# Performance work log

Hardware: AMD Instinct MI355X
Metric: run time of the kernel (lower is better)

## Reference

```python
import jax, jax.numpy as jnp
import numpy as np

NUM_USERS = 100_000
NUM_ITEMS = 50_000
EMBED_DIM = 64
NUM_LAYERS = 3
NUM_BASE_EDGES = 2_000_000
BATCH = 4096


def setup_inputs() -> dict:
    key = jax.random.key(0)
    k_ue, k_ie, k_u, k_i, k_uid, k_iid = jax.random.split(key, 6)
    N = NUM_USERS + NUM_ITEMS
    # learned embedding tables (std=0.01 init as in the torch module)
    user_emb = 0.01 * jax.random.normal(k_ue, (NUM_USERS, EMBED_DIM), dtype=jnp.float32)
    item_emb = 0.01 * jax.random.normal(k_ie, (NUM_ITEMS, EMBED_DIM), dtype=jnp.float32)
    # random bipartite interaction edges (u, v); symmetrized as in _build_graph
    u = jax.random.randint(k_u, (NUM_BASE_EDGES,), 0, NUM_USERS, dtype=jnp.int32)
    v = jax.random.randint(k_i, (NUM_BASE_EDGES,), 0, NUM_ITEMS, dtype=jnp.int32) + NUM_USERS
    rows = jnp.concatenate([u, v])  # [2E]
    cols = jnp.concatenate([v, u])  # [2E]
    # symmetric degree normalization: A_hat[r,c] = 1 / (sqrt(deg[r]) * sqrt(deg[c]))
    deg = jax.ops.segment_sum(jnp.ones_like(rows, dtype=jnp.float32), rows, num_segments=N)
    sqrt_deg = jnp.sqrt(deg)
    vals = 1.0 / (sqrt_deg[rows] * sqrt_deg[cols])
    user_ids = jax.random.randint(k_uid, (BATCH,), 0, NUM_USERS, dtype=jnp.int32)
    item_ids = jax.random.randint(k_iid, (BATCH,), 0, NUM_ITEMS, dtype=jnp.int32)
    return {
        "user_emb": user_emb,
        "item_emb": item_emb,
        "vals": vals,
        "rows": rows,
        "cols": cols,
        "user_ids": user_ids,
        "item_ids": item_ids,
    }


def _spmm(vals, rows, cols, x, num_segments):
    # COO SpMM: out[r] += vals[e] * x[cols[e]]  (irregular gather + scatter-add)
    return jax.ops.segment_sum(vals[:, None] * x[cols], rows, num_segments=num_segments)


def reference(user_emb, item_emb, vals, rows, cols, user_ids, item_ids):
    num_users = user_emb.shape[0]
    N = num_users + item_emb.shape[0]
    all_emb = jnp.concatenate([user_emb, item_emb], axis=0)  # [N, D]
    acc = jnp.zeros_like(all_emb)
    for _ in range(NUM_LAYERS):  # eval mode: no stochastic noise injection
        all_emb = _spmm(vals, rows, cols, all_emb, N)
        acc = acc + all_emb
    final = acc / NUM_LAYERS  # mean over layer outputs
    u = final[user_ids]                       # [B, D]
    i = final[item_ids + num_users]           # [B, D]
    return (u * i).sum(axis=-1)               # [B]
```

## Files before the change

kernel.cpp:

```cpp
#include <hip/hip_runtime.h>


#define EMBED_DIM 64
#define NUM_LAYERS 3
#define RSHIFT 8
#define RMASK 255
#define NBMAX 640
#define CAPU 8192
#define CAPI 12288
#define TP 3584
#define OUT_CAP 12288

__device__ __forceinline__ int bucket_base(int b, int BSPLIT) {
    int lo = (b < BSPLIT) ? b : BSPLIT;
    int hi = (b > BSPLIT) ? (b - BSPLIT) : 0;
    return lo * CAPU + hi * CAPI;
}


__device__ __forceinline__ unsigned bf16pair(float a, float b) {
    unsigned ia = __float_as_uint(a);
    unsigned ib = __float_as_uint(b);
    ia = (ia + 0x7fffu + ((ia >> 16) & 1u)) >> 16;
    ib = (ib + 0x7fffu + ((ib >> 16) & 1u)) & 0xffff0000u;
    return ia | ib;
}
__device__ __forceinline__ float bf_lo(unsigned u) { return __uint_as_float(u << 16); }
__device__ __forceinline__ float bf_hi(unsigned u) { return __uint_as_float(u & 0xffff0000u); }


__global__ __launch_bounds__(512) void split_kernel(const int* __restrict__ uu,
                                                    const int* __restrict__ vv,
                                                    int* __restrict__ gcur,
                                                    int* __restrict__ bin, int E2, int NB,
                                                    int BSPLIT) {
    __shared__ int h[NBMAX], exl[NBMAX], curb[NBMAX], gb[NBMAX];
    __shared__ int wp[8];
    __shared__ int stage[2 * TP];
    int tid = threadIdx.x;
    int lane = tid & 63, wid = tid >> 6;
    for (int i = tid; i < NB; i += 512) h[i] = 0;
    __syncthreads();
    int e0 = blockIdx.x * TP, e1 = min(e0 + TP, E2);
    int j = e0 + tid * 4;
    for (; j + 3 < e1; j += 2048) {
        int4 u4 = *(const int4*)(uu + j);
        int4 v4 = *(const int4*)(vv + j);
        atomicAdd(&h[u4.x >> RSHIFT], 1); atomicAdd(&h[v4.x >> RSHIFT], 1);
        atomicAdd(&h[u4.y >> RSHIFT], 1); atomicAdd(&h[v4.y >> RSHIFT], 1);
        atomicAdd(&h[u4.z >> RSHIFT], 1); atomicAdd(&h[v4.z >> RSHIFT], 1);
        atomicAdd(&h[u4.w >> RSHIFT], 1); atomicAdd(&h[v4.w >> RSHIFT], 1);
    }
    for (; j < e1; ++j) {
        atomicAdd(&h[uu[j] >> RSHIFT], 1);
        atomicAdd(&h[vv[j] >> RSHIFT], 1);
    }
    __syncthreads();
    {
        int b2 = tid * 2;
        int v0 = (b2     < NB) ? h[b2]     : 0;
        int v1 = (b2 + 1 < NB) ? h[b2 + 1] : 0;
        int tsum = v0 + v1;
        int x = tsum;
        for (int off = 1; off < 64; off <<= 1) {
            int y = __shfl_up(x, off, 64);
            if (lane >= off) x += y;
        }
        if (lane == 63) wp[wid] = x;
        __syncthreads();
        int wadd = 0;
        for (int k = 0; k < wid; ++k) wadd += wp[k];
        int tpre = wadd + x - tsum;
        if (b2     < NB) exl[b2]     = tpre;
        if (b2 + 1 < NB) exl[b2 + 1] = tpre + v0;
        __syncthreads();
    }
    for (int b = tid; b < NB; b += 512) {
        curb[b] = exl[b];
        gb[b]   = h[b] ? (bucket_base(b, BSPLIT) + atomicAdd(&gcur[b], h[b])) : 0;
    }
    __syncthreads();
    j = e0 + tid * 4;
    for (; j + 3 < e1; j += 2048) {
        int4 u4 = *(const int4*)(uu + j);
        int4 v4 = *(const int4*)(vv + j);
        int p;
        p = atomicAdd(&curb[u4.x >> RSHIFT], 1); stage[p] = (v4.x << RSHIFT) | (u4.x & RMASK);
        p = atomicAdd(&curb[v4.x >> RSHIFT], 1); stage[p] = (u4.x << RSHIFT) | (v4.x & RMASK);
        p = atomicAdd(&curb[u4.y >> RSHIFT], 1); stage[p] = (v4.y << RSHIFT) | (u4.y & RMASK);
        p = atomicAdd(&curb[v4.y >> RSHIFT], 1); stage[p] = (u4.y << RSHIFT) | (v4.y & RMASK);
        p = atomicAdd(&curb[u4.z >> RSHIFT], 1); stage[p] = (v4.z << RSHIFT) | (u4.z & RMASK);
        p = atomicAdd(&curb[v4.z >> RSHIFT], 1); stage[p] = (u4.z << RSHIFT) | (v4.z & RMASK);
        p = atomicAdd(&curb[u4.w >> RSHIFT], 1); stage[p] = (v4.w << RSHIFT) | (u4.w & RMASK);
        p = atomicAdd(&curb[v4.w >> RSHIFT], 1); stage[p] = (u4.w << RSHIFT) | (v4.w & RMASK);
    }
    for (; j < e1; ++j) {
        int u = uu[j], v = vv[j];
        int p1 = atomicAdd(&curb[u >> RSHIFT], 1);
        stage[p1] = (v << RSHIFT) | (u & RMASK);
        int p2 = atomicAdd(&curb[v >> RSHIFT], 1);
        stage[p2] = (u << RSHIFT) | (v & RMASK);
    }
    __syncthreads();
    int noct = tid >> 3, osub = tid & 7;
    for (int b = noct; b < NB; b += 64) {
        int cnt_b = h[b];
        int st = exl[b], g = gb[b];
        for (int k = osub; k < cnt_b; k += 8) bin[g + k] = stage[st + k];
    }
}


__global__ __launch_bounds__(512) void csr_kernel(const int* __restrict__ bin,
                                                  const int* __restrict__ gcur,
                                                  int* __restrict__ row_ptr,
                                                  int* __restrict__ deg,
                                                  int* __restrict__ col_idx,
                                                  const float4* __restrict__ ue,
                                                  const float4* __restrict__ ie,
                                                  unsigned* __restrict__ w0x,
                                                  int N, int U, int BSPLIT, int NB) {
    __shared__ int h2[256], cur2[256];
    __shared__ float rs2[256];
    __shared__ int wp[8];
    __shared__ __align__(16) int outst[OUT_CAP];
    int nbi = NB - BSPLIT;
    int bb  = blockIdx.x;
    int b   = (bb < nbi) ? (BSPLIT + bb) : (bb - nbi);
    int tid = threadIdx.x;
    int lane = tid & 63, wid = tid >> 6;
    int s = bucket_base(b, BSPLIT);
    int cnt = gcur[b];
    if (tid < 256) h2[tid] = 0;
    __syncthreads();
    int cnt4 = cnt >> 2;
    const int4* bin4 = (const int4*)(bin + s);
    for (int j = tid; j < cnt4; j += 512) {
        int4 v = bin4[j];
        atomicAdd(&h2[v.x & RMASK], 1);
        atomicAdd(&h2[v.y & RMASK], 1);
        atomicAdd(&h2[v.z & RMASK], 1);
        atomicAdd(&h2[v.w & RMASK], 1);
    }
    for (int j = (cnt4 << 2) + tid; j < cnt; j += 512) atomicAdd(&h2[bin[s + j] & RMASK], 1);
    __syncthreads();
    int myh = (tid < 256) ? h2[tid] : 0;
    if (tid < 256) rs2[tid] = (myh > 0) ? rsqrtf((float)myh) : 0.0f;
    {
        int x = myh;
        for (int off = 1; off < 64; off <<= 1) {
            int y = __shfl_up(x, off, 64);
            if (lane >= off) x += y;
        }
        if (lane == 63) wp[wid] = x;
        __syncthreads();
        if (tid < 256) {
            int wadd = 0;
            for (int k = 0; k < wid; ++k) wadd += wp[k];
            cur2[tid] = wadd + x - myh;
        }
    }
    int gr = (b << RSHIFT) + tid;
    if (tid < 256 && gr < N) {
        row_ptr[gr] = s + cur2[tid];
        deg[gr]     = myh;
    }
    __syncthreads();
    if (cnt <= OUT_CAP) {
        for (int j = tid; j < cnt4; j += 512) {
            int4 v = bin4[j];
            int p;
            p = atomicAdd(&cur2[v.x & RMASK], 1); outst[p] = v.x >> RSHIFT;
            p = atomicAdd(&cur2[v.y & RMASK], 1); outst[p] = v.y >> RSHIFT;
            p = atomicAdd(&cur2[v.z & RMASK], 1); outst[p] = v.z >> RSHIFT;
            p = atomicAdd(&cur2[v.w & RMASK], 1); outst[p] = v.w >> RSHIFT;
        }
        for (int j = (cnt4 << 2) + tid; j < cnt; j += 512) {
            int v = bin[s + j];
            int p = atomicAdd(&cur2[v & RMASK], 1);
            outst[p] = v >> RSHIFT;
        }
        __syncthreads();
        int4* dst4 = (int4*)(col_idx + s);
        for (int j = tid; j < cnt4; j += 512) dst4[j] = ((const int4*)outst)[j];
        for (int j = (cnt4 << 2) + tid; j < cnt; j += 512) col_idx[s + j] = outst[j];
    } else {
        for (int j = tid; j < cnt; j += 512) {
            int v = bin[s + j];
            int p = atomicAdd(&cur2[v & RMASK], 1);
            col_idx[s + p] = v >> RSHIFT;
        }
    }
    for (int idx = tid; idx < 256 * 16; idx += 512) {
        int rl = idx >> 4, sub = idx & 15;
        int n = (b << RSHIFT) + rl;
        if (n < N) {
            float4 v = (n < U) ? ue[(size_t)n * 16 + sub] : ie[(size_t)(n - U) * 16 + sub];
            float rs = rs2[rl];
            uint2 o;
            o.x = bf16pair(v.x * rs, v.y * rs);
            o.y = bf16pair(v.z * rs, v.w * rs);
            ((uint2*)w0x)[(size_t)n * 16 + sub] = o;
        }
    }
}


__global__ __launch_bounds__(256) void spmm_kernel(const int* __restrict__ row_ptr,
                                                   const int* __restrict__ deg,
                                                   const int* __restrict__ col_idx,
                                                   const uint4* __restrict__ x4,
                                                   uint4* __restrict__ y4, int N) {
    int gw   = (blockIdx.x * blockDim.x + threadIdx.x) >> 6;
    int lane = threadIdx.x & 63;
    int oct  = lane >> 3, sub = lane & 7;
    int r = gw * 8 + oct;
    if (r >= N) return;
    int s = row_ptr[r];
    int d = deg[r];
    float2 a0 = {0, 0}, a1 = {0, 0}, a2 = {0, 0}, a3 = {0, 0};
    int k = 0;
    for (; k + 3 < d; k += 4) {
        int c0 = col_idx[s + k];
        int c1 = col_idx[s + k + 1];
        int c2 = col_idx[s + k + 2];
        int c3 = col_idx[s + k + 3];
        uint4 u0 = x4[(size_t)c0 * 8 + sub];
        uint4 u1 = x4[(size_t)c1 * 8 + sub];
        uint4 u2 = x4[(size_t)c2 * 8 + sub];
        uint4 u3 = x4[(size_t)c3 * 8 + sub];
        a0.x += bf_lo(u0.x); a0.y += bf_hi(u0.x);
        a1.x += bf_lo(u0.y); a1.y += bf_hi(u0.y);
        a2.x += bf_lo(u0.z); a2.y += bf_hi(u0.z);
        a3.x += bf_lo(u0.w); a3.y += bf_hi(u0.w);
        a0.x += bf_lo(u1.x); a0.y += bf_hi(u1.x);
        a1.x += bf_lo(u1.y); a1.y += bf_hi(u1.y);
        a2.x += bf_lo(u1.z); a2.y += bf_hi(u1.z);
        a3.x += bf_lo(u1.w); a3.y += bf_hi(u1.w);
        a0.x += bf_lo(u2.x); a0.y += bf_hi(u2.x);
        a1.x += bf_lo(u2.y); a1.y += bf_hi(u2.y);
        a2.x += bf_lo(u2.z); a2.y += bf_hi(u2.z);
        a3.x += bf_lo(u2.w); a3.y += bf_hi(u2.w);
        a0.x += bf_lo(u3.x); a0.y += bf_hi(u3.x);
        a1.x += bf_lo(u3.y); a1.y += bf_hi(u3.y);
        a2.x += bf_lo(u3.z); a2.y += bf_hi(u3.z);
        a3.x += bf_lo(u3.w); a3.y += bf_hi(u3.w);
    }
    for (; k < d; ++k) {
        int c0 = col_idx[s + k];
        uint4 u0 = x4[(size_t)c0 * 8 + sub];
        a0.x += bf_lo(u0.x); a0.y += bf_hi(u0.x);
        a1.x += bf_lo(u0.y); a1.y += bf_hi(u0.y);
        a2.x += bf_lo(u0.z); a2.y += bf_hi(u0.z);
        a3.x += bf_lo(u0.w); a3.y += bf_hi(u0.w);
    }
    float inv = (d > 0) ? (1.0f / (float)d) : 0.0f;
    uint4 o;
    o.x = bf16pair(a0.x * inv, a0.y * inv);
    o.y = bf16pair(a1.x * inv, a1.y * inv);
    o.z = bf16pair(a2.x * inv, a2.y * inv);
    o.w = bf16pair(a3.x * inv, a3.y * inv);
    y4[(size_t)r * 8 + sub] = o;
}


__global__ __launch_bounds__(128) void batch_readout_kernel(const int* __restrict__ row_ptr,
                                                            const int* __restrict__ deg,
                                                            const int* __restrict__ col_idx,
                                                            const uint4* __restrict__ x4,
                                                            const uint4* __restrict__ l1,
                                                            const uint4* __restrict__ l2,
                                                            const int* __restrict__ user_ids,
                                                            const int* __restrict__ item_ids,
                                                            float* __restrict__ out,
                                                            int B, int U) {
    __shared__ float sm[8][8][8];
    __shared__ float dsm[8];
    int tid = threadIdx.x;
    int oct = tid >> 3, sub = tid & 7;
    int pair = oct & 7, is_item = oct >> 3;
    int b = blockIdx.x * 8 + pair;
    bool active = (b < B);
    float sv[8];
#pragma unroll
    for (int k = 0; k < 8; ++k) sv[k] = 0.0f;
    float dd = 0.0f;
    if (active) {
        int r = is_item ? (item_ids[b] + U) : user_ids[b];
        int s = row_ptr[r];
        int d = deg[r];
        dd = (float)d;
        float2 a0 = {0, 0}, a1 = {0, 0}, a2 = {0, 0}, a3 = {0, 0};
        int k = 0;
        for (; k + 3 < d; k += 4) {
            int c0 = col_idx[s + k];
            int c1 = col_idx[s + k + 1];
            int c2 = col_idx[s + k + 2];
            int c3 = col_idx[s + k + 3];
            uint4 u0 = x4[(size_t)c0 * 8 + sub];
            uint4 u1 = x4[(size_t)c1 * 8 + sub];
            uint4 u2 = x4[(size_t)c2 * 8 + sub];
            uint4 u3 = x4[(size_t)c3 * 8 + sub];
            a0.x += bf_lo(u0.x); a0.y += bf_hi(u0.x);
            a1.x += bf_lo(u0.y); a1.y += bf_hi(u0.y);
            a2.x += bf_lo(u0.z); a2.y += bf_hi(u0.z);
            a3.x += bf_lo(u0.w); a3.y += bf_hi(u0.w);
            a0.x += bf_lo(u1.x); a0.y += bf_hi(u1.x);
            a1.x += bf_lo(u1.y); a1.y += bf_hi(u1.y);
            a2.x += bf_lo(u1.z); a2.y += bf_hi(u1.z);
            a3.x += bf_lo(u1.w); a3.y += bf_hi(u1.w);
            a0.x += bf_lo(u2.x); a0.y += bf_hi(u2.x);
            a1.x += bf_lo(u2.y); a1.y += bf_hi(u2.y);
            a2.x += bf_lo(u2.z); a2.y += bf_hi(u2.z);
            a3.x += bf_lo(u2.w); a3.y += bf_hi(u2.w);
            a0.x += bf_lo(u3.x); a0.y += bf_hi(u3.x);
            a1.x += bf_lo(u3.y); a1.y += bf_hi(u3.y);
            a2.x += bf_lo(u3.z); a2.y += bf_hi(u3.z);
            a3.x += bf_lo(u3.w); a3.y += bf_hi(u3.w);
        }
        for (; k < d; ++k) {
            int c0 = col_idx[s + k];
            uint4 u0 = x4[(size_t)c0 * 8 + sub];
            a0.x += bf_lo(u0.x); a0.y += bf_hi(u0.x);
            a1.x += bf_lo(u0.y); a1.y += bf_hi(u0.y);
            a2.x += bf_lo(u0.z); a2.y += bf_hi(u0.z);
            a3.x += bf_lo(u0.w); a3.y += bf_hi(u0.w);
        }
        float inv = (d > 0) ? (1.0f / (float)d) : 0.0f;
        uint4 u1v = l1[(size_t)r * 8 + sub];
        uint4 u2v = l2[(size_t)r * 8 + sub];
        sv[0] = bf_lo(u1v.x) + bf_lo(u2v.x) + a0.x * inv;
        sv[1] = bf_hi(u1v.x) + bf_hi(u2v.x) + a0.y * inv;
        sv[2] = bf_lo(u1v.y) + bf_lo(u2v.y) + a1.x * inv;
        sv[3] = bf_hi(u1v.y) + bf_hi(u2v.y) + a1.y * inv;
        sv[4] = bf_lo(u1v.z) + bf_lo(u2v.z) + a2.x * inv;
        sv[5] = bf_hi(u1v.z) + bf_hi(u2v.z) + a2.y * inv;
        sv[6] = bf_lo(u1v.w) + bf_lo(u2v.w) + a3.x * inv;
        sv[7] = bf_hi(u1v.w) + bf_hi(u2v.w) + a3.y * inv;
    }
    if (is_item) {
#pragma unroll
        for (int k = 0; k < 8; ++k) sm[pair][sub][k] = sv[k];
        if (sub == 0) dsm[pair] = dd;
    }
    __syncthreads();
    if (!is_item && active) {
        float p = 0.0f;
#pragma unroll
        for (int k = 0; k < 8; ++k) p += sv[k] * sm[pair][sub][k];
#pragma unroll
        for (int off = 4; off > 0; off >>= 1) p += __shfl_down(p, off, 8);
        if (sub == 0) {
            float du = dd;
            float di = dsm[pair];
            out[b] = p * sqrtf(du) * sqrtf(di) * (1.0f / (NUM_LAYERS * NUM_LAYERS));
        }
    }
}


extern "C" void kernel_launch(void* const* d_in, const int* in_sizes, int n_in,
                              void* d_out, int out_size, void* d_ws, size_t ws_size,
                              hipStream_t stream) {
    const float* user_emb = (const float*)d_in[0];
    const float* item_emb = (const float*)d_in[1];
    const int*   rows     = (const int*)d_in[3];
    const int*   cols     = (const int*)d_in[4];
    const int*   user_ids = (const int*)d_in[5];
    const int*   item_ids = (const int*)d_in[6];
    float*       out      = (float*)d_out;

    const int U = in_sizes[0] / EMBED_DIM;
    const int I = in_sizes[1] / EMBED_DIM;
    const int E2 = in_sizes[3] >> 1;
    const int B = in_sizes[5];
    const int N = U + I;
    const int NB = (N + RMASK) >> RSHIFT;
    const int BSPLIT = U >> RSHIFT;

    const long long TOT = (long long)((NB < BSPLIT ? NB : BSPLIT)) * CAPU +
                          (long long)((NB > BSPLIT) ? (NB - BSPLIT) : 0) * CAPI;

    char* w = (char*)d_ws;
    unsigned* x2      = (unsigned*)w; w += (size_t)N * 32 * sizeof(unsigned);
    unsigned* L1      = (unsigned*)w; w += (size_t)N * 32 * sizeof(unsigned);
    unsigned* L2      = (unsigned*)w; w += (size_t)N * 32 * sizeof(unsigned);
    int*      bin     = (int*)w;      w += (size_t)TOT * sizeof(int);
    int*      col_idx = (int*)w;      w += (size_t)TOT * sizeof(int);
    int*      row_ptr = (int*)w;      w += (size_t)N * sizeof(int);
    int*      deg     = (int*)w;      w += (size_t)N * sizeof(int);
    int*      gcur    = (int*)w;      w += (size_t)NB * sizeof(int);

    const int GP = (E2 + TP - 1) / TP;

    hipMemsetAsync(gcur, 0, (size_t)NB * sizeof(int), stream);
    split_kernel<<<GP, 512, 0, stream>>>(rows, cols, gcur, bin, E2, NB, BSPLIT);
    csr_kernel<<<NB, 512, 0, stream>>>(bin, gcur, row_ptr, deg, col_idx,
                                       (const float4*)user_emb, (const float4*)item_emb,
                                       x2, N, U, BSPLIT, NB);

    const int T = 256;
    const int GS = (N * 8 + T - 1) / T;
    spmm_kernel<<<GS, T, 0, stream>>>(row_ptr, deg, col_idx,
                                      (const uint4*)x2, (uint4*)L1, N);
    spmm_kernel<<<GS, T, 0, stream>>>(row_ptr, deg, col_idx,
                                      (const uint4*)L1, (uint4*)L2, N);

    batch_readout_kernel<<<(B + 7) / 8, 128, 0, stream>>>(row_ptr, deg, col_idx,
                                                          (const uint4*)L2,
                                                          (const uint4*)L1, (const uint4*)L2,
                                                          user_ids, item_ids, out, B, U);
}
```

Baseline: 287.5 us.

## Pack row_ptr and degree into int2, double split/csr block size and tile

Merges the separate row_ptr and deg arrays into one interleaved int2 array, so SpMM and readout fetch each row's start and degree with a single 8-byte load. Also doubles the split kernel's edge tile and raises the split and CSR kernels to 1024 threads, which halves the number of split blocks and the global atomics on bucket cursors. The split prefix scan now uses one bin per thread. Larger blocks with bigger shared staging may lower occupancy.

```diff
diff --git a/kernel.cpp b/kernel.cpp
--- a/kernel.cpp
+++ b/kernel.cpp
@@ -8,7 +8,7 @@
 #define NBMAX 640
 #define CAPU 8192
 #define CAPI 12288
-#define TP 3584
+#define TP 7168
 #define OUT_CAP 12288
 
 __device__ __forceinline__ int bucket_base(int b, int BSPLIT) {
@@ -29,21 +29,21 @@
 __device__ __forceinline__ float bf_hi(unsigned u) { return __uint_as_float(u & 0xffff0000u); }
 
 
-__global__ __launch_bounds__(512) void split_kernel(const int* __restrict__ uu,
-                                                    const int* __restrict__ vv,
-                                                    int* __restrict__ gcur,
-                                                    int* __restrict__ bin, int E2, int NB,
-                                                    int BSPLIT) {
+__global__ __launch_bounds__(1024) void split_kernel(const int* __restrict__ uu,
+                                                     const int* __restrict__ vv,
+                                                     int* __restrict__ gcur,
+                                                     int* __restrict__ bin, int E2, int NB,
+                                                     int BSPLIT) {
     __shared__ int h[NBMAX], exl[NBMAX], curb[NBMAX], gb[NBMAX];
-    __shared__ int wp[8];
+    __shared__ int wp[16];
     __shared__ int stage[2 * TP];
     int tid = threadIdx.x;
     int lane = tid & 63, wid = tid >> 6;
-    for (int i = tid; i < NB; i += 512) h[i] = 0;
+    for (int i = tid; i < NB; i += 1024) h[i] = 0;
     __syncthreads();
     int e0 = blockIdx.x * TP, e1 = min(e0 + TP, E2);
     int j = e0 + tid * 4;
-    for (; j + 3 < e1; j += 2048) {
+    for (; j + 3 < e1; j += 4096) {
         int4 u4 = *(const int4*)(uu + j);
         int4 v4 = *(const int4*)(vv + j);
         atomicAdd(&h[u4.x >> RSHIFT], 1); atomicAdd(&h[v4.x >> RSHIFT], 1);
@@ -57,11 +57,8 @@
     }
     __syncthreads();
     {
-        int b2 = tid * 2;
-        int v0 = (b2     < NB) ? h[b2]     : 0;
-        int v1 = (b2 + 1 < NB) ? h[b2 + 1] : 0;
-        int tsum = v0 + v1;
-        int x = tsum;
+        int v0 = (tid < NB) ? h[tid] : 0;
+        int x = v0;
         for (int off = 1; off < 64; off <<= 1) {
             int y = __shfl_up(x, off, 64);
             if (lane >= off) x += y;
@@ -70,18 +67,16 @@
         __syncthreads();
         int wadd = 0;
         for (int k = 0; k < wid; ++k) wadd += wp[k];
-        int tpre = wadd + x - tsum;
-        if (b2     < NB) exl[b2]     = tpre;
-        if (b2 + 1 < NB) exl[b2 + 1] = tpre + v0;
+        if (tid < NB) exl[tid] = wadd + x - v0;
         __syncthreads();
     }
-    for (int b = tid; b < NB; b += 512) {
+    for (int b = tid; b < NB; b += 1024) {
         curb[b] = exl[b];
         gb[b]   = h[b] ? (bucket_base(b, BSPLIT) + atomicAdd(&gcur[b], h[b])) : 0;
     }
     __syncthreads();
     j = e0 + tid * 4;
-    for (; j + 3 < e1; j += 2048) {
+    for (; j + 3 < e1; j += 4096) {
         int4 u4 = *(const int4*)(uu + j);
         int4 v4 = *(const int4*)(vv + j);
         int p;
@@ -103,7 +98,7 @@
     }
     __syncthreads();
     int noct = tid >> 3, osub = tid & 7;
-    for (int b = noct; b < NB; b += 64) {
+    for (int b = noct; b < NB; b += 128) {
         int cnt_b = h[b];
         int st = exl[b], g = gb[b];
         for (int k = osub; k < cnt_b; k += 8) bin[g + k] = stage[st + k];
@@ -111,18 +106,17 @@
 }
 
 
-__global__ __launch_bounds__(512) void csr_kernel(const int* __restrict__ bin,
-                                                  const int* __restrict__ gcur,
-                                                  int* __restrict__ row_ptr,
-                                                  int* __restrict__ deg,
-                                                  int* __restrict__ col_idx,
-                                                  const float4* __restrict__ ue,
-                                                  const float4* __restrict__ ie,
-                                                  unsigned* __restrict__ w0x,
-                                                  int N, int U, int BSPLIT, int NB) {
+__global__ __launch_bounds__(1024) void csr_kernel(const int* __restrict__ bin,
+                                                   const int* __restrict__ gcur,
+                                                   int2* __restrict__ rpd,
+                                                   int* __restrict__ col_idx,
+                                                   const float4* __restrict__ ue,
+                                                   const float4* __restrict__ ie,
+                                                   unsigned* __restrict__ w0x,
+                                                   int N, int U, int BSPLIT, int NB) {
     __shared__ int h2[256], cur2[256];
     __shared__ float rs2[256];
-    __shared__ int wp[8];
+    __shared__ int wp[16];
     __shared__ __align__(16) int outst[OUT_CAP];
     int nbi = NB - BSPLIT;
     int bb  = blockIdx.x;
@@ -135,14 +129,14 @@
     __syncthreads();
     int cnt4 = cnt >> 2;
     const int4* bin4 = (const int4*)(bin + s);
-    for (int j = tid; j < cnt4; j += 512) {
+    for (int j = tid; j < cnt4; j += 1024) {
         int4 v = bin4[j];
         atomicAdd(&h2[v.x & RMASK], 1);
         atomicAdd(&h2[v.y & RMASK], 1);
         atomicAdd(&h2[v.z & RMASK], 1);
         atomicAdd(&h2[v.w & RMASK], 1);
     }
-    for (int j = (cnt4 << 2) + tid; j < cnt; j += 512) atomicAdd(&h2[bin[s + j] & RMASK], 1);
+    for (int j = (cnt4 << 2) + tid; j < cnt; j += 1024) atomicAdd(&h2[bin[s + j] & RMASK], 1);
     __syncthreads();
     int myh = (tid < 256) ? h2[tid] : 0;
     if (tid < 256) rs2[tid] = (myh > 0) ? rsqrtf((float)myh) : 0.0f;
@@ -162,12 +156,12 @@
     }
     int gr = (b << RSHIFT) + tid;
     if (tid < 256 && gr < N) {
-        row_ptr[gr] = s + cur2[tid];
-        deg[gr]     = myh;
+        int2 v; v.x = s + cur2[tid]; v.y = myh;
+        rpd[gr] = v;
     }
     __syncthreads();
     if (cnt <= OUT_CAP) {
-        for (int j = tid; j < cnt4; j += 512) {
+        for (int j = tid; j < cnt4; j += 1024) {
             int4 v = bin4[j];
             int p;
             p = atomicAdd(&cur2[v.x & RMASK], 1); outst[p] = v.x >> RSHIFT;
@@ -175,23 +169,23 @@
             p = atomicAdd(&cur2[v.z & RMASK], 1); outst[p] = v.z >> RSHIFT;
             p = atomicAdd(&cur2[v.w & RMASK], 1); outst[p] = v.w >> RSHIFT;
         }
-        for (int j = (cnt4 << 2) + tid; j < cnt; j += 512) {
+        for (int j = (cnt4 << 2) + tid; j < cnt; j += 1024) {
             int v = bin[s + j];
             int p = atomicAdd(&cur2[v & RMASK], 1);
             outst[p] = v >> RSHIFT;
         }
         __syncthreads();
         int4* dst4 = (int4*)(col_idx + s);
-        for (int j = tid; j < cnt4; j += 512) dst4[j] = ((const int4*)outst)[j];
-        for (int j = (cnt4 << 2) + tid; j < cnt; j += 512) col_idx[s + j] = outst[j];
+        for (int j = tid; j < cnt4; j += 1024) dst4[j] = ((const int4*)outst)[j];
+        for (int j = (cnt4 << 2) + tid; j < cnt; j += 1024) col_idx[s + j] = outst[j];
     } else {
-        for (int j = tid; j < cnt; j += 512) {
+        for (int j = tid; j < cnt; j += 1024) {
             int v = bin[s + j];
             int p = atomicAdd(&cur2[v & RMASK], 1);
             col_idx[s + p] = v >> RSHIFT;
         }
     }
-    for (int idx = tid; idx < 256 * 16; idx += 512) {
+    for (int idx = tid; idx < 256 * 16; idx += 1024) {
         int rl = idx >> 4, sub = idx & 15;
         int n = (b << RSHIFT) + rl;
         if (n < N) {
@@ -206,8 +200,7 @@
 }
 
 
-__global__ __launch_bounds__(256) void spmm_kernel(const int* __restrict__ row_ptr,
-                                                   const int* __restrict__ deg,
+__global__ __launch_bounds__(256) void spmm_kernel(const int2* __restrict__ rpd,
                                                    const int* __restrict__ col_idx,
                                                    const uint4* __restrict__ x4,
                                                    uint4* __restrict__ y4, int N) {
@@ -216,8 +209,9 @@
     int oct  = lane >> 3, sub = lane & 7;
     int r = gw * 8 + oct;
     if (r >= N) return;
-    int s = row_ptr[r];
-    int d = deg[r];
+    int2 rd = rpd[r];
+    int s = rd.x;
+    int d = rd.y;
     float2 a0 = {0, 0}, a1 = {0, 0}, a2 = {0, 0}, a3 = {0, 0};
     int k = 0;
     for (; k + 3 < d; k += 4) {
@@ -264,8 +258,7 @@
 }
 
 
-__global__ __launch_bounds__(128) void batch_readout_kernel(const int* __restrict__ row_ptr,
-                                                            const int* __restrict__ deg,
+__global__ __launch_bounds__(128) void batch_readout_kernel(const int2* __restrict__ rpd,
                                                             const int* __restrict__ col_idx,
                                                             const uint4* __restrict__ x4,
                                                             const uint4* __restrict__ l1,
@@ -287,8 +280,9 @@
     float dd = 0.0f;
     if (active) {
         int r = is_item ? (item_ids[b] + U) : user_ids[b];
-        int s = row_ptr[r];
-        int d = deg[r];
+        int2 rd = rpd[r];
+        int s = rd.x;
+        int d = rd.y;
         dd = (float)d;
         float2 a0 = {0, 0}, a1 = {0, 0}, a2 = {0, 0}, a3 = {0, 0};
         int k = 0;
@@ -387,26 +381,23 @@
     unsigned* L2      = (unsigned*)w; w += (size_t)N * 32 * sizeof(unsigned);
     int*      bin     = (int*)w;      w += (size_t)TOT * sizeof(int);
     int*      col_idx = (int*)w;      w += (size_t)TOT * sizeof(int);
-    int*      row_ptr = (int*)w;      w += (size_t)N * sizeof(int);
-    int*      deg     = (int*)w;      w += (size_t)N * sizeof(int);
+    int2*     rpd     = (int2*)w;     w += (size_t)N * sizeof(int2);
     int*      gcur    = (int*)w;      w += (size_t)NB * sizeof(int);
 
     const int GP = (E2 + TP - 1) / TP;
 
     hipMemsetAsync(gcur, 0, (size_t)NB * sizeof(int), stream);
-    split_kernel<<<GP, 512, 0, stream>>>(rows, cols, gcur, bin, E2, NB, BSPLIT);
-    csr_kernel<<<NB, 512, 0, stream>>>(bin, gcur, row_ptr, deg, col_idx,
-                                       (const float4*)user_emb, (const float4*)item_emb,
-                                       x2, N, U, BSPLIT, NB);
+    split_kernel<<<GP, 1024, 0, stream>>>(rows, cols, gcur, bin, E2, NB, BSPLIT);
+    csr_kernel<<<NB, 1024, 0, stream>>>(bin, gcur, rpd, col_idx,
+                                        (const float4*)user_emb, (const float4*)item_emb,
+                                        x2, N, U, BSPLIT, NB);
 
     const int T = 256;
     const int GS = (N * 8 + T - 1) / T;
-    spmm_kernel<<<GS, T, 0, stream>>>(row_ptr, deg, col_idx,
-                                      (const uint4*)x2, (uint4*)L1, N);
-    spmm_kernel<<<GS, T, 0, stream>>>(row_ptr, deg, col_idx,
-                                      (const uint4*)L1, (uint4*)L2, N);
-
-    batch_readout_kernel<<<(B + 7) / 8, 128, 0, stream>>>(row_ptr, deg, col_idx,
+    spmm_kernel<<<GS, T, 0, stream>>>(rpd, col_idx, (const uint4*)x2, (uint4*)L1, N);
+    spmm_kernel<<<GS, T, 0, stream>>>(rpd, col_idx, (const uint4*)L1, (uint4*)L2, N);
+
+    batch_readout_kernel<<<(B + 7) / 8, 128, 0, stream>>>(rpd, col_idx,
                                                           (const uint4*)L2,
                                                           (const uint4*)L1, (const uint4*)L2,
                                                           user_ids, item_ids, out, B, U);
```

Measured after the change: 283.7 us, median of 2. About the same (-1.3%).
